# Kernel tuning notes

Hardware: AMD Instinct MI355X
Metric: run time of the kernel (lower is better)

## Reference

```python
import jax, jax.numpy as jnp
import numpy as np

G = 50000            # number of 5-node crystal graphs
NPG = 5              # nodes per graph (forward reshapes to (-1, 5, F))
N = G * NPG          # total nodes
IN = 64              # in_size (61 atomic-number feats + 3 position)
OUT = 64             # out_size
HID = 2 * OUT        # hidden width per __init__


def setup_inputs() -> dict:
    key = jax.random.key(0)
    ks = jax.random.split(key, 8)
    h = jax.random.normal(ks[0], (N, IN - 3), jnp.float32)
    x = jax.random.normal(ks[1], (N, 3), jnp.float32)
    # complete graph with self-loops inside each 5-node crystal
    base = np.arange(G, dtype=np.int64) * NPG
    li = np.repeat(np.arange(NPG, dtype=np.int64), NPG)
    lj = np.tile(np.arange(NPG, dtype=np.int64), NPG)
    src = jnp.asarray((base[:, None] + li[None, :]).reshape(-1))
    dst = jnp.asarray((base[:, None] + lj[None, :]).reshape(-1))

    def lin(k, fi, fo):
        return jax.random.normal(k, (fi, fo), jnp.float32) / np.float32(np.sqrt(fi))

    W1 = lin(ks[2], IN, HID);  b1 = jnp.zeros((HID,), jnp.float32)
    W2 = lin(ks[3], HID, HID); b2 = jnp.zeros((HID,), jnp.float32)
    W3 = lin(ks[4], HID, HID); b3 = jnp.zeros((HID,), jnp.float32)
    W4 = lin(ks[5], HID, OUT); b4 = jnp.zeros((OUT,), jnp.float32)
    return {"h": h, "x": x, "src": src, "dst": dst,
            "W1": W1, "b1": b1, "W2": W2, "b2": b2,
            "W3": W3, "b3": b3, "W4": W4, "b4": b4}


def _graph_conv(feat, src, dst, W, b):
    # DGL GraphConv, norm='both': D_dst^{-1/2} A D_src^{-1/2} X W + b
    e = src.shape[0]
    ones = jnp.ones((e,), feat.dtype)
    deg_out = jax.ops.segment_sum(ones, src, num_segments=N)
    deg_in = jax.ops.segment_sum(ones, dst, num_segments=N)
    norm_src = jax.lax.rsqrt(jnp.maximum(deg_out, 1.0))
    norm_dst = jax.lax.rsqrt(jnp.maximum(deg_in, 1.0))
    norm_e = norm_src[src] * norm_dst[dst]                      # [E]
    agg = jax.ops.segment_sum(feat[src] * norm_e[:, None], dst,
                              num_segments=N)                   # [N, F]
    return agg @ W + b


def reference(h, x, src, dst, W1, b1, W2, b2, W3, b3, W4, b4):
    hx = jnp.concatenate([h, x.astype(jnp.float32)], axis=1)   # [N, IN]
    f1 = _graph_conv(hx, src, dst, W1, b1)
    f2 = _graph_conv(f1, src, dst, W2, b2)
    f3 = _graph_conv(f2, src, dst, W3, b3)
    f4 = _graph_conv(f3, src, dst, W4, b4)                      # [N, OUT]
    return jnp.mean(f4.reshape((-1, NPG, f4.shape[-1])), axis=1)  # [G, OUT]
```

## Files before the change

### kernel.cpp

```cpp
#include <hip/hip_runtime.h>


#define WCQOFF 16640
#define BCOFF  20736
#define GB 16
#define NTILE 2

__global__ void __launch_bounds__(256) collapseX(
    const float* __restrict__ W1, const float* __restrict__ b1,
    const float* __restrict__ W2, const float* __restrict__ b2,
    const float* __restrict__ W3, const float* __restrict__ b3,
    const float* __restrict__ W4, const float* __restrict__ b4,
    float* __restrict__ ws) {
  __shared__ float red[512];
  __shared__ float arow[128];
  __shared__ float trow[128];

  const int tid = threadIdx.x, wv = tid >> 6, lane = tid & 63;
  const int r = blockIdx.x;

  if (r < 64) {
    {
      const int kb = wv * 32;
      const float* w1p = W1 + r * 128 + kb;
      const float* w2p = W2 + kb * 128;
      float p0 = 0.f, p1 = 0.f;
      #pragma unroll 8
      for (int kk = 0; kk < 32; ++kk) {
        float w1 = w1p[kk];
        p0 += w1 * w2p[kk * 128 + lane];
        p1 += w1 * w2p[kk * 128 + lane + 64];
      }
      red[wv * 128 + lane] = p0;
      red[wv * 128 + lane + 64] = p1;
    }
    __syncthreads();
    if (tid < 128) arow[tid] = red[tid] + red[128 + tid] + red[256 + tid] + red[384 + tid];
    __syncthreads();

    {
      const int kb = wv * 32;
      const float* w3p = W3 + kb * 128;
      float p0 = 0.f, p1 = 0.f;
      #pragma unroll 8
      for (int kk = 0; kk < 32; ++kk) {
        float a = arow[kb + kk];
        p0 += a * w3p[kk * 128 + lane];
        p1 += a * w3p[kk * 128 + lane + 64];
      }
      red[wv * 128 + lane] = p0;
      red[wv * 128 + lane + 64] = p1;
    }
    __syncthreads();
    if (tid < 128) trow[tid] = red[tid] + red[128 + tid] + red[256 + tid] + red[384 + tid];
    __syncthreads();

    {
      const int kb = wv * 32;
      const float* w4p = W4 + kb * 64;
      float p = 0.f;
      #pragma unroll 8
      for (int kk = 0; kk < 32; ++kk) p += trow[kb + kk] * w4p[kk * 64 + lane];
      red[wv * 128 + lane] = p;
    }
    __syncthreads();
    if (tid < 64) {
      float wc = red[tid] + red[128 + tid] + red[256 + tid] + red[384 + tid];
      ws[WCQOFF + (r >> 2) * 256 + tid * 4 + (r & 3)] = wc * 0.2f;
    }
  } else {
    if (tid < 128) {
      float s = b2[tid];
      #pragma unroll 4
      for (int k = 0; k < 128; ++k) s += b1[k] * W2[k * 128 + tid];
      arow[tid] = s;
    }
    __syncthreads();
    if (tid < 128) {
      float s = b3[tid];
      #pragma unroll 4
      for (int k = 0; k < 128; ++k) s += arow[k] * W3[k * 128 + tid];
      trow[tid] = s;
    }
    __syncthreads();
    if (tid < 64) {
      float s = b4[tid];
      #pragma unroll 4
      for (int k = 0; k < 128; ++k) s += trow[k] * W4[k * 64 + tid];
      ws[BCOFF + tid] = s;
    }
  }
}

__global__ void __launch_bounds__(256) gcn_main(
    const float* __restrict__ h, const float* __restrict__ x,
    const float* __restrict__ ws, float* __restrict__ out, int G) {
  __shared__ __align__(16) float Ws[4096];
  __shared__ __align__(16) float m_s[4][4][64];

  int tid = threadIdx.x, wv = tid >> 6, lane = tid & 63;
  float bco = ws[BCOFF + lane];

  {
    const float4* src = (const float4*)(ws + WCQOFF);
    float4* dst = (float4*)Ws;
    #pragma unroll
    for (int i = 0; i < 4; ++i) dst[tid + 256 * i] = src[tid + 256 * i];
  }

  bool ish = lane < 61;
  long st = ish ? 61 : 3;
  bool did_bar = false;

  #pragma unroll 1
  for (int t = 0; t < NTILE; ++t) {
    long tile = (long)blockIdx.x * NTILE + t;
    long gbase = tile * GB + (long)wv * 4;
    if (gbase >= G) break;

    float sv[4];
    #pragma unroll
    for (int j = 0; j < 4; ++j) {
      long g = gbase + j;
      if (g < G) {
        const float* p = ish ? (h + g * 305 + lane) : (x + g * 15 + (lane - 61));
        sv[j] = __builtin_nontemporal_load(p) +
                __builtin_nontemporal_load(p + st) +
                __builtin_nontemporal_load(p + 2 * st) +
                __builtin_nontemporal_load(p + 3 * st) +
                __builtin_nontemporal_load(p + 4 * st);
      } else sv[j] = 0.f;
    }
    #pragma unroll
    for (int j = 0; j < 4; ++j) m_s[wv][j][lane] = sv[j];

    if (!did_bar) { __syncthreads(); did_bar = true; }

    {
      const float4* Wl = (const float4*)Ws;
      const float4* m0 = (const float4*)&m_s[wv][0][0];
      const float4* m1 = (const float4*)&m_s[wv][1][0];
      const float4* m2 = (const float4*)&m_s[wv][2][0];
      const float4* m3 = (const float4*)&m_s[wv][3][0];
      float a0 = bco, a1 = bco, a2 = bco, a3 = bco;
      #pragma unroll 4
      for (int q = 0; q < 16; ++q) {
        float4 w = Wl[q * 64 + lane];
        float4 v0 = m0[q], v1 = m1[q], v2 = m2[q], v3 = m3[q];
        a0 += v0.x * w.x + v0.y * w.y + v0.z * w.z + v0.w * w.w;
        a1 += v1.x * w.x + v1.y * w.y + v1.z * w.z + v1.w * w.w;
        a2 += v2.x * w.x + v2.y * w.y + v2.z * w.z + v2.w * w.w;
        a3 += v3.x * w.x + v3.y * w.y + v3.z * w.z + v3.w * w.w;
      }
      long ob = gbase * 64 + lane;
      if (gbase + 0 < G) __builtin_nontemporal_store(a0, &out[ob + 0]);
      if (gbase + 1 < G) __builtin_nontemporal_store(a1, &out[ob + 64]);
      if (gbase + 2 < G) __builtin_nontemporal_store(a2, &out[ob + 128]);
      if (gbase + 3 < G) __builtin_nontemporal_store(a3, &out[ob + 192]);
    }
  }
}

extern "C" void kernel_launch(void* const* d_in, const int* in_sizes, int n_in,
                              void* d_out, int out_size, void* d_ws, size_t ws_size,
                              hipStream_t stream) {
  const float* h  = (const float*)d_in[0];
  const float* x  = (const float*)d_in[1];
  const float* W1 = (const float*)d_in[4];
  const float* b1 = (const float*)d_in[5];
  const float* W2 = (const float*)d_in[6];
  const float* b2 = (const float*)d_in[7];
  const float* W3 = (const float*)d_in[8];
  const float* b3 = (const float*)d_in[9];
  const float* W4 = (const float*)d_in[10];
  const float* b4 = (const float*)d_in[11];
  float* ws = (float*)d_ws;
  float* out = (float*)d_out;

  int G = in_sizes[0] / 305;

  collapseX<<<65, 256, 0, stream>>>(W1, b1, W2, b2, W3, b3, W4, b4, ws);
  int tiles = (G + GB - 1) / GB;
  int blocks = (tiles + NTILE - 1) / NTILE;
  gcn_main<<<blocks, 256, 0, stream>>>(h, x, ws, out, G);
}
```

Baseline: 35.29 us.

## Use bf16 MFMA for the collapsed weight matmul in the main kernel

Result: faster. 34.30 us (-2.8%).

```diff
diff --git a/kernel.cpp b/kernel.cpp
--- a/kernel.cpp
+++ b/kernel.cpp
@@ -1,10 +1,19 @@
 #include <hip/hip_runtime.h>
 
 
-#define WCQOFF 16640
 #define BCOFF  20736
+#define WTOFF  24576
 #define GB 16
 #define NTILE 2
+
+typedef __attribute__((ext_vector_type(8))) short short8;
+typedef __attribute__((ext_vector_type(4))) float f32x4;
+
+__device__ __forceinline__ unsigned short f2bf(float f) {
+  unsigned u = __float_as_uint(f);
+  u += 0x7FFFu + ((u >> 16) & 1u);
+  return (unsigned short)(u >> 16);
+}
 
 __global__ void __launch_bounds__(256) collapseX(
     const float* __restrict__ W1, const float* __restrict__ b1,
@@ -66,7 +75,7 @@
     __syncthreads();
     if (tid < 64) {
       float wc = red[tid] + red[128 + tid] + red[256 + tid] + red[384 + tid];
-      ws[WCQOFF + (r >> 2) * 256 + tid * 4 + (r & 3)] = wc * 0.2f;
+      ((unsigned short*)(ws + WTOFF))[tid * 64 + r] = f2bf(wc * 0.2f);
     }
   } else {
     if (tid < 128) {
@@ -95,69 +104,67 @@
 __global__ void __launch_bounds__(256) gcn_main(
     const float* __restrict__ h, const float* __restrict__ x,
     const float* __restrict__ ws, float* __restrict__ out, int G) {
-  __shared__ __align__(16) float Ws[4096];
-  __shared__ __align__(16) float m_s[4][4][64];
+  __shared__ __align__(16) unsigned short wt_u16[64 * 72];
+  __shared__ __align__(16) unsigned short m_u16[16 * 72];
 
   int tid = threadIdx.x, wv = tid >> 6, lane = tid & 63;
-  float bco = ws[BCOFF + lane];
+  int ntiles = (G + GB - 1) / GB;
 
-  {
-    const float4* src = (const float4*)(ws + WCQOFF);
-    float4* dst = (float4*)Ws;
+  float bcv = ws[BCOFF + wv * 16 + (lane & 15)];
+
+  if (tid < 64) {
+    const float4* src = (const float4*)((const unsigned short*)(ws + WTOFF) + tid * 64);
+    float4* dst = (float4*)&wt_u16[tid * 72];
     #pragma unroll
-    for (int i = 0; i < 4; ++i) dst[tid + 256 * i] = src[tid + 256 * i];
+    for (int j = 0; j < 8; ++j) dst[j] = src[j];
   }
 
   bool ish = lane < 61;
   long st = ish ? 61 : 3;
-  bool did_bar = false;
 
   #pragma unroll 1
   for (int t = 0; t < NTILE; ++t) {
     long tile = (long)blockIdx.x * NTILE + t;
-    long gbase = tile * GB + (long)wv * 4;
-    if (gbase >= G) break;
+    if (tile >= ntiles) break;
+    long tb = tile * GB;
+    long gbase = tb + (long)wv * 4;
 
-    float sv[4];
     #pragma unroll
     for (int j = 0; j < 4; ++j) {
       long g = gbase + j;
+      float sv = 0.f;
       if (g < G) {
         const float* p = ish ? (h + g * 305 + lane) : (x + g * 15 + (lane - 61));
-        sv[j] = __builtin_nontemporal_load(p) +
-                __builtin_nontemporal_load(p + st) +
-                __builtin_nontemporal_load(p + 2 * st) +
-                __builtin_nontemporal_load(p + 3 * st) +
-                __builtin_nontemporal_load(p + 4 * st);
-      } else sv[j] = 0.f;
+        sv = __builtin_nontemporal_load(p) +
+             __builtin_nontemporal_load(p + st) +
+             __builtin_nontemporal_load(p + 2 * st) +
+             __builtin_nontemporal_load(p + 3 * st) +
+             __builtin_nontemporal_load(p + 4 * st);
+      }
+      m_u16[(wv * 4 + j) * 72 + lane] = f2bf(sv);
     }
-    #pragma unroll
-    for (int j = 0; j < 4; ++j) m_s[wv][j][lane] = sv[j];
 
-    if (!did_bar) { __syncthreads(); did_bar = true; }
+    __syncthreads();
 
     {
-      const float4* Wl = (const float4*)Ws;
-      const float4* m0 = (const float4*)&m_s[wv][0][0];
-      const float4* m1 = (const float4*)&m_s[wv][1][0];
-      const float4* m2 = (const float4*)&m_s[wv][2][0];
-      const float4* m3 = (const float4*)&m_s[wv][3][0];
-      float a0 = bco, a1 = bco, a2 = bco, a3 = bco;
-      #pragma unroll 4
-      for (int q = 0; q < 16; ++q) {
-        float4 w = Wl[q * 64 + lane];
-        float4 v0 = m0[q], v1 = m1[q], v2 = m2[q], v3 = m3[q];
-        a0 += v0.x * w.x + v0.y * w.y + v0.z * w.z + v0.w * w.w;
-        a1 += v1.x * w.x + v1.y * w.y + v1.z * w.z + v1.w * w.w;
-        a2 += v2.x * w.x + v2.y * w.y + v2.z * w.z + v2.w * w.w;
-        a3 += v3.x * w.x + v3.y * w.y + v3.z * w.z + v3.w * w.w;
+      int m = lane & 15, k8 = lane >> 4;
+      const short8 a0 = *(const short8*)&m_u16[m * 72 + k8 * 8];
+      const short8 a1 = *(const short8*)&m_u16[m * 72 + 32 + k8 * 8];
+      const short8 b0 = *(const short8*)&wt_u16[(wv * 16 + m) * 72 + k8 * 8];
+      const short8 b1 = *(const short8*)&wt_u16[(wv * 16 + m) * 72 + 32 + k8 * 8];
+      f32x4 acc = {bcv, bcv, bcv, bcv};
+      acc = __builtin_amdgcn_mfma_f32_16x16x32_bf16(a0, b0, acc, 0, 0, 0);
+      acc = __builtin_amdgcn_mfma_f32_16x16x32_bf16(a1, b1, acc, 0, 0, 0);
+
+      int n = wv * 16 + (lane & 15);
+      #pragma unroll
+      for (int r = 0; r < 4; ++r) {
+        long g = tb + (lane >> 4) * 4 + r;
+        if (g < G) __builtin_nontemporal_store(acc[r], &out[g * 64 + n]);
       }
-      long ob = gbase * 64 + lane;
-      if (gbase + 0 < G) __builtin_nontemporal_store(a0, &out[ob + 0]);
-      if (gbase + 1 < G) __builtin_nontemporal_store(a1, &out[ob + 64]);
-      if (gbase + 2 < G) __builtin_nontemporal_store(a2, &out[ob + 128]);
-      if (gbase + 3 < G) __builtin_nontemporal_store(a3, &out[ob + 192]);
     }
+
+    __syncthreads();
   }
 }
 
```
